# Optimization experiments

Hardware: AMD Instinct MI355X
Metric: run time of the kernel (lower is better)

The kernel has to match this reference:

```python
import jax, jax.numpy as jnp
import numpy as np

B, J, O = 32, 20, 20
D, H, F, L = 256, 8, 1024, 6
S = J * O
DH = D // H
NL = L + 1  # 6 encoder blocks + final block stacked together


def setup_inputs() -> dict:
    ks = jax.random.split(jax.random.key(0), 16)
    s = 0.02
    am = jax.random.randint(ks[4], (B, J), 0, 2) == 1
    am = am.at[:, 0].set(False)  # at least one unmasked job per row (avoid all -inf softmax)
    return {
        "operations": jax.random.normal(ks[0], (B, J, O, 2), jnp.float32),
        "job_ops_mask": jax.random.normal(ks[1], (B, J, O, O), jnp.float32),
        "ops_machines_mask": jax.random.normal(ks[2], (B, S, S), jnp.float32),
        "jobs_next_op_idx": jax.random.randint(ks[3], (B, J, 1), 0, O),
        "action_mask": am,
        "qkv_w": jax.random.normal(ks[5], (NL, 3 * D, D), jnp.float32) * s,
        "qkv_b": jnp.zeros((NL, 3 * D), jnp.float32),
        "out_w": jax.random.normal(ks[6], (NL, D, D), jnp.float32) * s,
        "out_b": jnp.zeros((NL, D), jnp.float32),
        "ln1_g": jnp.ones((NL, D), jnp.float32),
        "ln1_b": jnp.zeros((NL, D), jnp.float32),
        "ln2_g": jnp.ones((NL, D), jnp.float32),
        "ln2_b": jnp.zeros((NL, D), jnp.float32),
        "ff1_w": jax.random.normal(ks[7], (NL, F, D), jnp.float32) * s,
        "ff1_b": jnp.zeros((NL, F), jnp.float32),
        "ff2_w": jax.random.normal(ks[8], (NL, D, F), jnp.float32) * s,
        "ff2_b": jnp.zeros((NL, D), jnp.float32),
        "op_emb_w": jax.random.normal(ks[9], (D, 2), jnp.float32) * s,
        "op_emb_b": jnp.zeros((D,), jnp.float32),
        "pol_w": jax.random.normal(ks[10], (1, D), jnp.float32) * s,
        "pol_b": jnp.zeros((1,), jnp.float32),
    }


def _ln(x, g, b):
    m = x.mean(-1, keepdims=True)
    v = ((x - m) ** 2).mean(-1, keepdims=True)
    return (x - m) * jax.lax.rsqrt(v + 1e-5) * g + b


def _mha(x, mask, qw, qb, ow, ob):
    N, Sq, _ = x.shape
    qkv = x @ qw.T + qb
    q, k, v = jnp.split(qkv, 3, axis=-1)
    q = q.reshape(N, Sq, H, DH).transpose(0, 2, 1, 3)
    k = k.reshape(N, Sq, H, DH).transpose(0, 2, 1, 3)
    v = v.reshape(N, Sq, H, DH).transpose(0, 2, 1, 3)
    sc = jnp.einsum("nhqd,nhkd->nhqk", q, k) / jnp.sqrt(jnp.float32(DH))
    sc = sc + mask  # additive float attn mask, broadcast over heads where needed
    a = jax.nn.softmax(sc, axis=-1)
    o = jnp.einsum("nhqk,nhkd->nhqd", a, v).transpose(0, 2, 1, 3).reshape(N, Sq, D)
    return o @ ow.T + ob


def _forward(operations, job_ops_mask, ops_machines_mask, jobs_next_op_idx, action_mask,
             qkv_w, qkv_b, out_w, out_b, ln1_g, ln1_b, ln2_g, ln2_b,
             ff1_w, ff1_b, ff2_w, ff2_b, op_emb_w, op_emb_b, pol_w, pol_b):
    def block(x, mask, i):  # pre-norm TransformerEncoderLayer, gelu, dropout=0
        h = _ln(x, ln1_g[i], ln1_b[i])
        x = x + _mha(h, mask, qkv_w[i], qkv_b[i], out_w[i], out_b[i])
        h = _ln(x, ln2_g[i], ln2_b[i])
        ff = jax.nn.gelu(h @ ff1_w[i].T + ff1_b[i], approximate=False) @ ff2_w[i].T + ff2_b[i]
        return x + ff

    # sinusoidal positional encoding over the operation index
    pos = jnp.arange(O, dtype=jnp.float32)[:, None]
    div = jnp.exp(jnp.arange(0, D, 2, dtype=jnp.float32) * (-np.log(10000.0) / D))
    pe = jnp.stack([jnp.sin(pos * div), jnp.cos(pos * div)], axis=-1).reshape(O, D)
    x = operations @ op_emb_w.T + op_emb_b + pe[None, None]  # (B,J,O,D)

    # ALiBi slopes: 1/x^(i+1), x = 256^(1/H)
    base = (2.0 ** 8) ** (1.0 / H)
    slope = (1.0 / base ** jnp.arange(1, H + 1, dtype=jnp.float32))[None, :, None, None]
    job_mask = job_ops_mask.reshape(B * J, 1, O, O) * slope  # (B*J, H, O, O)
    mach_mask = ops_machines_mask[:, None, :, :]  # (B, 1, S, S), identical across heads

    for i in range(L):
        if i % 2 == 0:  # per-job attention over operations
            x = block(x.reshape(B * J, O, D), job_mask, i).reshape(B, J, O, D)
        else:  # per-machine attention over all operations
            x = block(x.reshape(B, S, D), mach_mask, i).reshape(B, J, O, D)

    idx = jnp.broadcast_to(jobs_next_op_idx[:, :, :, None], (B, J, 1, D))
    nxt = jnp.take_along_axis(x, idx, axis=2)[:, :, 0, :]  # (B, J, D)
    kp = jnp.where(action_mask, -jnp.inf, 0.0)[:, None, None, :]  # key padding mask
    nxt = block(nxt, kp, L)
    logits = (nxt @ pol_w.T + pol_b)[:, :, 0]
    return jnp.where(action_mask, -jnp.inf, logits)


def reference(operations, job_ops_mask, ops_machines_mask, jobs_next_op_idx, action_mask,
              qkv_w, qkv_b, out_w, out_b, ln1_g, ln1_b, ln2_g, ln2_b,
              ff1_w, ff1_b, ff2_w, ff2_b, op_emb_w, op_emb_b, pol_w, pol_b):
    return _forward(operations, job_ops_mask, ops_machines_mask, jobs_next_op_idx, action_mask,
                    qkv_w, qkv_b, out_w, out_b, ln1_g, ln1_b, ln2_g, ln2_b,
                    ff1_w, ff1_b, ff2_w, ff2_b, op_emb_w, op_emb_b, pol_w, pol_b)
```

## Files before the change

kernel.cpp:

```cpp
#include <hip/hip_runtime.h>
#include <math.h>

#define B_  32
#define J_  20
#define O_  20
#define S_  400
#define D_  256
#define H_  8
#define F_  1024
#define L_  6
#define T_  12800
#define T2_ 640

#define NEG_BIG (-1e30f)

typedef __attribute__((ext_vector_type(8))) short short8;
typedef __attribute__((ext_vector_type(4))) float f32x4;

__device__ __forceinline__ short f2b(float f) {
  union { float f; unsigned u; } c; c.f = f;
  unsigned r = (c.u + 0x7FFFu + ((c.u >> 16) & 1u)) >> 16;
  return (short)r;
}
__device__ __forceinline__ float b2f(short s) {
  union { unsigned u; float f; } c;
  c.u = ((unsigned)(unsigned short)s) << 16;
  return c.f;
}
__device__ __forceinline__ unsigned addpk(unsigned a, unsigned b) {
  union { unsigned u; float f; } x, y;
  x.u = a << 16;        y.u = b << 16;        float lo = x.f + y.f;
  x.u = a & 0xffff0000u; y.u = b & 0xffff0000u; float hi = x.f + y.f;
  return (unsigned)(unsigned short)f2b(lo) | ((unsigned)(unsigned short)f2b(hi) << 16);
}
__device__ __forceinline__ void async_copy16(const short* g, short* l) {
  __builtin_amdgcn_global_load_lds(
      (const __attribute__((address_space(1))) void*)g,
      (__attribute__((address_space(3))) void*)l, 16, 0, 0);
}

__global__ __launch_bounds__(256) void k_f2b4(
    const float* __restrict__ s0, short* __restrict__ d0,
    const float* __restrict__ s1, short* __restrict__ d1,
    const float* __restrict__ s2, short* __restrict__ d2,
    const float* __restrict__ s3, short* __restrict__ d3,
    const float* __restrict__ s4, short* __restrict__ d4)
{
  int bid = blockIdx.x;
  const float* src; short* dst; int base;
  if (bid < 672)        { src = s0; dst = d0; base = bid; }
  else if (bid < 896)   { src = s1; dst = d1; base = bid - 672; }
  else if (bid < 1792)  { src = s2; dst = d2; base = bid - 896; }
  else if (bid < 2688)  { src = s3; dst = d3; base = bid - 1792; }
  else                  { src = s4; dst = d4; base = bid - 2688; }
  int i = (base * 256 + threadIdx.x) * 8;
  float4 a = *(const float4*)(src + i);
  float4 b = *(const float4*)(src + i + 4);
  short8 o;
  o[0] = f2b(a.x); o[1] = f2b(a.y); o[2] = f2b(a.z); o[3] = f2b(a.w);
  o[4] = f2b(b.x); o[5] = f2b(b.y); o[6] = f2b(b.z); o[7] = f2b(b.w);
  *(short8*)(dst + i) = o;
}

__global__ __launch_bounds__(640) void k_maskconv(
    const void* __restrict__ am_raw, int* __restrict__ am_out)
{
  __shared__ int isInt32;
  const int tid = threadIdx.x;
  if (tid == 0) isInt32 = 1;
  __syncthreads();
  if (tid < 160) {
    int v = ((const int*)am_raw)[tid];
    if (v != 0 && v != 1) atomicAnd(&isInt32, 0);
  }
  __syncthreads();
  if (tid < 640) {
    int v;
    if (isInt32) v = ((const int*)am_raw)[tid] != 0;
    else         v = ((const unsigned char*)am_raw)[tid] != 0;
    am_out[tid] = v;
  }
}

__global__ __launch_bounds__(256) void k_embed(
    const float* __restrict__ ops, const float* __restrict__ ew,
    const float* __restrict__ eb, short* __restrict__ x)
{
  int idx = blockIdx.x * 256 + threadIdx.x;
  int d = idx & 255;
  int t = idx >> 8;
  int o = t % O_;
  float a0 = ops[(size_t)t * 2 + 0], a1 = ops[(size_t)t * 2 + 1];
  int k = d >> 1;
  float div = expf((float)(2 * k) * -0.03597789207803197f);
  float ang = (float)o * div;
  float pe = (d & 1) ? cosf(ang) : sinf(ang);
  x[idx] = f2b(a0 * ew[d * 2 + 0] + a1 * ew[d * 2 + 1] + eb[d] + pe);
}

__global__ __launch_bounds__(256) void k_ln(
    const short* __restrict__ x, const float* __restrict__ g, const float* __restrict__ b,
    short* __restrict__ out, int nTok)
{
  int gid = blockIdx.x * 256 + threadIdx.x;
  int tok = gid >> 6, lane = threadIdx.x & 63;
  if (tok >= nTok) return;
  int2 pk = ((const int2*)(x + (size_t)tok * 256))[lane];
  union { unsigned u; float f; } c;
  float vx, vy, vz, vw;
  c.u = (unsigned)pk.x << 16;        vx = c.f;
  c.u = (unsigned)pk.x & 0xffff0000u; vy = c.f;
  c.u = (unsigned)pk.y << 16;        vz = c.f;
  c.u = (unsigned)pk.y & 0xffff0000u; vw = c.f;
  float s = vx + vy + vz + vw;
  #pragma unroll
  for (int off = 32; off > 0; off >>= 1) s += __shfl_down(s, off);
  float mean = __shfl(s, 0) * (1.f / 256.f);
  float dx = vx - mean, dy = vy - mean, dz = vz - mean, dw = vw - mean;
  float q = dx * dx + dy * dy + dz * dz + dw * dw;
  #pragma unroll
  for (int off = 32; off > 0; off >>= 1) q += __shfl_down(q, off);
  float var = __shfl(q, 0) * (1.f / 256.f);
  float inv = 1.f / sqrtf(var + 1e-5f);
  float4 gv = ((const float4*)g)[lane];
  float4 bv = ((const float4*)b)[lane];
  float ox = dx * inv * gv.x + bv.x;
  float oy = dy * inv * gv.y + bv.y;
  float oz = dz * inv * gv.z + bv.z;
  float ow = dw * inv * gv.w + bv.w;
  int2 po;
  po.x = (int)(unsigned short)f2b(ox) | ((int)(unsigned short)f2b(oy) << 16);
  po.y = (int)(unsigned short)f2b(oz) | ((int)(unsigned short)f2b(ow) << 16);
  ((int2*)(out + (size_t)tok * 256))[lane] = po;
}

__global__ __launch_bounds__(256) void k_gemm_bf16(
    const short* __restrict__ A, const short* __restrict__ W,
    const float* __restrict__ bias, const short* __restrict__ R,
    short* __restrict__ C, int M, int N, int K, int act)
{
  __shared__ short LDS_[17408];
  short* Asf = LDS_;
  short* Bsf = LDS_ + 8192;
  short* Csf = LDS_;
  const int tid  = threadIdx.x;
  const int lane = tid & 63;
  const int wv   = tid >> 6;
  const int lm   = lane & 15;
  const int quad = lane >> 4;
  const int wm   = (wv >> 1) * 64;
  const int wn   = (wv & 1) * 64;
  const int n0 = blockIdx.x * 128;
  const int m0 = blockIdx.y * 128;

  f32x4 acc[4][4] = {};

  for (int k0 = 0; k0 < K; k0 += 64) {
    __syncthreads();
    #pragma unroll
    for (int i = 0; i < 4; ++i) {
      const int c    = tid + 256 * i;
      const int row  = c >> 3;
      const int kc8  = ((c & 7) ^ (row & 7)) * 8;
      async_copy16(A + (size_t)(m0 + row) * K + k0 + kc8, &Asf[c * 8]);
      async_copy16(W + (size_t)(n0 + row) * K + k0 + kc8, &Bsf[c * 8]);
    }
    __syncthreads();
    #pragma unroll
    for (int kh = 0; kh < 2; ++kh) {
      short8 af[4], bf[4];
      #pragma unroll
      for (int i = 0; i < 4; ++i) {
        const int row  = wm + i * 16 + lm;
        const int slot = (kh * 4 + quad) ^ (lm & 7);
        af[i] = *(short8*)&Asf[(row * 8 + slot) * 8];
      }
      #pragma unroll
      for (int j = 0; j < 4; ++j) {
        const int row  = wn + j * 16 + lm;
        const int slot = (kh * 4 + quad) ^ (lm & 7);
        bf[j] = *(short8*)&Bsf[(row * 8 + slot) * 8];
      }
      #pragma unroll
      for (int i = 0; i < 4; ++i)
        #pragma unroll
        for (int j = 0; j < 4; ++j)
          acc[i][j] = __builtin_amdgcn_mfma_f32_16x16x32_bf16(af[i], bf[j], acc[i][j], 0, 0, 0);
    }
  }

  __syncthreads();
  #pragma unroll
  for (int j = 0; j < 4; ++j) {
    const int ccol = wn + j * 16 + lm;
    const float bv = bias[n0 + ccol];
    #pragma unroll
    for (int i = 0; i < 4; ++i) {
      #pragma unroll
      for (int r = 0; r < 4; ++r) {
        const int row = wm + i * 16 + quad * 4 + r;
        float vvv = acc[i][j][r] + bv;
        if (act) vvv = vvv / (1.f + __expf(-1.702f * vvv));
        Csf[row * 136 + ccol] = f2b(vvv);
      }
    }
  }
  __syncthreads();
  {
    const int srow = tid >> 1, sh = (tid & 1) * 64;
    const size_t gbase = (size_t)(m0 + srow) * N + n0 + sh;
    const short* ls = &Csf[srow * 136 + sh];
    #pragma unroll
    for (int u = 0; u < 8; ++u) {
      uint4 v = *(const uint4*)(ls + u * 8);
      if (R) {
        uint4 rv = *(const uint4*)(R + gbase + u * 8);
        v.x = addpk(v.x, rv.x); v.y = addpk(v.y, rv.y);
        v.z = addpk(v.z, rv.z); v.w = addpk(v.w, rv.w);
      }
      *(uint4*)(C + gbase + u * 8) = v;
    }
  }
}

__global__ __launch_bounds__(256) void k_gemm_ln(
    const short* __restrict__ A, const short* __restrict__ W,
    const float* __restrict__ bias, const short* __restrict__ R,
    short* __restrict__ X, short* __restrict__ Hout,
    const float* __restrict__ g, const float* __restrict__ bb_,
    int M, int K)
{
  __shared__ short LDS_[4096 + 16896];
  short* Asf = LDS_;
  short* Bsf = LDS_ + 4096;
  short* Csf = LDS_ + 4096;
  const int tid  = threadIdx.x;
  const int lane = tid & 63;
  const int wv   = tid >> 6;
  const int lm   = lane & 15;
  const int quad = lane >> 4;
  const int wn   = wv * 64;
  const int m0   = blockIdx.x * 64;

  f32x4 acc[4][4] = {};

  for (int k0 = 0; k0 < K; k0 += 64) {
    __syncthreads();
    #pragma unroll
    for (int i = 0; i < 2; ++i) {
      const int c   = tid + 256 * i;
      const int row = c >> 3;
      const int kc8 = ((c & 7) ^ (row & 7)) * 8;
      async_copy16(A + (size_t)(m0 + row) * K + k0 + kc8, &Asf[c * 8]);
    }
    #pragma unroll
    for (int i = 0; i < 8; ++i) {
      const int c   = tid + 256 * i;
      const int row = c >> 3;
      const int kc8 = ((c & 7) ^ (row & 7)) * 8;
      async_copy16(W + (size_t)row * K + k0 + kc8, &Bsf[c * 8]);
    }
    __syncthreads();
    #pragma unroll
    for (int kh = 0; kh < 2; ++kh) {
      short8 af[4], bf[4];
      #pragma unroll
      for (int i = 0; i < 4; ++i) {
        const int row  = i * 16 + lm;
        const int slot = (kh * 4 + quad) ^ (lm & 7);
        af[i] = *(short8*)&Asf[(row * 8 + slot) * 8];
      }
      #pragma unroll
      for (int j = 0; j < 4; ++j) {
        const int row  = wn + j * 16 + lm;
        const int slot = (kh * 4 + quad) ^ (lm & 7);
        bf[j] = *(short8*)&Bsf[(row * 8 + slot) * 8];
      }
      #pragma unroll
      for (int i = 0; i < 4; ++i)
        #pragma unroll
        for (int j = 0; j < 4; ++j)
          acc[i][j] = __builtin_amdgcn_mfma_f32_16x16x32_bf16(af[i], bf[j], acc[i][j], 0, 0, 0);
    }
  }

  __syncthreads();
  #pragma unroll
  for (int j = 0; j < 4; ++j) {
    const int ccol = wn + j * 16 + lm;
    const float bv = bias[ccol];
    #pragma unroll
    for (int i = 0; i < 4; ++i) {
      #pragma unroll
      for (int r = 0; r < 4; ++r) {
        const int row = i * 16 + quad * 4 + r;
        Csf[row * 264 + ccol] = f2b(acc[i][j][r] + bv);
      }
    }
  }
  __syncthreads();

  {
    const int row = tid >> 2, cb = (tid & 3) * 64;
    const size_t gbase = (size_t)(m0 + row) * 256 + cb;
    const short* ls = &Csf[row * 264 + cb];
    uint4 xv[8];
    float s1 = 0.f, s2 = 0.f;
    #pragma unroll
    for (int u = 0; u < 8; ++u) {
      uint4 v = *(const uint4*)(ls + u * 8);
      uint4 rv = *(const uint4*)(R + gbase + u * 8);
      v.x = addpk(v.x, rv.x); v.y = addpk(v.y, rv.y);
      v.z = addpk(v.z, rv.z); v.w = addpk(v.w, rv.w);
      xv[u] = v;
      *(uint4*)(X + gbase + u * 8) = v;
      #pragma unroll
      for (int w2 = 0; w2 < 4; ++w2) {
        unsigned pv = (&v.x)[w2];
        union { unsigned u; float f; } c1, c2;
        c1.u = pv << 16; c2.u = pv & 0xffff0000u;
        s1 += c1.f + c2.f;
        s2 += c1.f * c1.f + c2.f * c2.f;
      }
    }
    s1 += __shfl_xor(s1, 1); s2 += __shfl_xor(s2, 1);
    s1 += __shfl_xor(s1, 2); s2 += __shfl_xor(s2, 2);
    const float mean = s1 * (1.f / 256.f);
    const float var  = s2 * (1.f / 256.f) - mean * mean;
    const float inv  = 1.f / sqrtf(var + 1e-5f);
    #pragma unroll
    for (int u = 0; u < 8; ++u) {
      float4 g0 = *(const float4*)(g + cb + u * 8);
      float4 g1 = *(const float4*)(g + cb + u * 8 + 4);
      float4 b0 = *(const float4*)(bb_ + cb + u * 8);
      float4 b1 = *(const float4*)(bb_ + cb + u * 8 + 4);
      auto lnpk = [&](unsigned pv, float ga, float gb2, float ba, float bb2) -> unsigned {
        union { unsigned u; float f; } c1, c2;
        c1.u = pv << 16; c2.u = pv & 0xffff0000u;
        float lo = (c1.f - mean) * inv * ga + ba;
        float hi = (c2.f - mean) * inv * gb2 + bb2;
        return (unsigned)(unsigned short)f2b(lo) | ((unsigned)(unsigned short)f2b(hi) << 16);
      };
      uint4 hv;
      hv.x = lnpk(xv[u].x, g0.x, g0.y, b0.x, b0.y);
      hv.y = lnpk(xv[u].y, g0.z, g0.w, b0.z, b0.w);
      hv.z = lnpk(xv[u].z, g1.x, g1.y, b1.x, b1.y);
      hv.w = lnpk(xv[u].w, g1.z, g1.w, b1.z, b1.w);
      *(uint4*)(Hout + gbase + u * 8) = hv;
    }
  }
}

#define QSTR 776
#define PSTR20 40
__global__ __launch_bounds__(512) void k_attn20_mfma(
    const short* __restrict__ qkv, short* __restrict__ att,
    const float* __restrict__ jmask, const int* __restrict__ amask, int mode)
{
  __shared__ short QK[32 * QSTR];
  __shared__ short Ps[8][32 * PSTR20];
  const int seq  = blockIdx.x;
  const int tid  = threadIdx.x;
  const int wv   = tid >> 6;
  const int lane = tid & 63;
  const int l15  = lane & 15;
  const int quad = lane >> 4;
  const float scale = 0.1767766952966369f;

  for (int e = tid; e < 3072; e += 512) {
    int row = e / 96, c8 = (e % 96) * 8;
    uint4 v = {0u, 0u, 0u, 0u};
    if (row < 20) v = *(const uint4*)(qkv + ((size_t)seq * 20 + row) * 768 + c8);
    *(uint4*)&QK[row * QSTR + c8] = v;
  }
  __syncthreads();

  const short8 aq0 = *(short8*)&QK[(0  + l15) * QSTR + wv * 32 + quad * 8];
  const short8 aq1 = *(short8*)&QK[(16 + l15) * QSTR + wv * 32 + quad * 8];
  const short8 bk0 = *(short8*)&QK[(0  + l15) * QSTR + 256 + wv * 32 + quad * 8];
  const short8 bk1 = *(short8*)&QK[(16 + l15) * QSTR + 256 + wv * 32 + quad * 8];
  f32x4 z4 = {0.f, 0.f, 0.f, 0.f};
  f32x4 s00 = __builtin_amdgcn_mfma_f32_16x16x32_bf16(aq0, bk0, z4, 0, 0, 0);
  f32x4 s01 = __builtin_amdgcn_mfma_f32_16x16x32_bf16(aq0, bk1, z4, 0, 0, 0);
  f32x4 s10 = __builtin_amdgcn_mfma_f32_16x16x32_bf16(aq1, bk0, z4, 0, 0, 0);
  f32x4 s11 = __builtin_amdgcn_mfma_f32_16x16x32_bf16(aq1, bk1, z4, 0, 0, 0);

  const float slope = exp2f(-(float)(wv + 1));
  short* psw = &Ps[wv][0];
  float l0[4] = {0.f, 0.f, 0.f, 0.f};
  float l1[4] = {0.f, 0.f, 0.f, 0.f};

  #pragma unroll
  for (int kt = 0; kt < 2; ++kt) {
    const int k  = kt * 16 + l15;
    const int kc = (k < 20) ? k : 19;
    float madd1 = 0.f;
    if (mode == 1) madd1 = amask[seq * 20 + kc] ? NEG_BIG : 0.f;
    #pragma unroll
    for (int qt = 0; qt < 2; ++qt) {
      f32x4 s = (kt == 0) ? (qt == 0 ? s00 : s10) : (qt == 0 ? s01 : s11);
      #pragma unroll
      for (int r = 0; r < 4; ++r) {
        const int q  = qt * 16 + quad * 4 + r;
        const int qc = (q < 20) ? q : 19;
        float sv = s[r] * scale;
        if (mode == 0) sv += jmask[(size_t)seq * 400 + qc * 20 + kc] * slope;
        else           sv += madd1;
        float p = (k < 20) ? __expf(fminf(sv, 40.f)) : 0.f;
        if (qt == 0) l0[r] += p; else l1[r] += p;
        psw[q * PSTR20 + k] = f2b(p);
      }
    }
  }
  #pragma unroll
  for (int r = 0; r < 4; ++r) {
    float t0 = l0[r];
    t0 += __shfl_xor(t0, 1); t0 += __shfl_xor(t0, 2);
    t0 += __shfl_xor(t0, 4); t0 += __shfl_xor(t0, 8);
    l0[r] = 1.f / t0;
    float t1 = l1[r];
    t1 += __shfl_xor(t1, 1); t1 += __shfl_xor(t1, 2);
    t1 += __shfl_xor(t1, 4); t1 += __shfl_xor(t1, 8);
    l1[r] = 1.f / t1;
  }

  const short8 pf0 = *(short8*)&psw[(0  + l15) * PSTR20 + quad * 8];
  const short8 pf1 = *(short8*)&psw[(16 + l15) * PSTR20 + quad * 8];
  #pragma unroll
  for (int dt = 0; dt < 2; ++dt) {
    const int d = wv * 32 + dt * 16 + l15;
    short8 vf;
    #pragma unroll
    for (int j = 0; j < 8; ++j)
      vf[j] = QK[(quad * 8 + j) * QSTR + 512 + d];
    f32x4 o0 = __builtin_amdgcn_mfma_f32_16x16x32_bf16(pf0, vf, z4, 0, 0, 0);
    f32x4 o1 = __builtin_amdgcn_mfma_f32_16x16x32_bf16(pf1, vf, z4, 0, 0, 0);
    #pragma unroll
    for (int r = 0; r < 4; ++r) {
      const int q = quad * 4 + r;
      att[((size_t)seq * 20 + q) * 256 + d] = f2b(o0[r] * l0[r]);
    }
    if (quad == 0) {
      #pragma unroll
      for (int r = 0; r < 4; ++r) {
        const int q = 16 + r;
        att[((size_t)seq * 20 + q) * 256 + d] = f2b(o1[r] * l1[r]);
      }
    }
  }
}

#define VTS 416
__global__ __launch_bounds__(256) void k_vtrans(
    const short* __restrict__ qkv, short* __restrict__ vt)
{
  __shared__ short T[64][73];
  const int bid = blockIdx.x;
  const int b  = bid / 28, rem = bid % 28;
  const int kt = rem / 4, dt = rem % 4;
  const int k0 = kt * 64, d0 = dt * 64;
  const int tid = threadIdx.x;
  #pragma unroll
  for (int i = 0; i < 2; ++i) {
    const int c = tid + 256 * i;
    const int row = c >> 3, cc = (c & 7) * 8;
    const int tok = k0 + row;
    uint4 v = {0u, 0u, 0u, 0u};
    if (tok < 400)
      v = *(const uint4*)(qkv + ((size_t)(b * 400 + tok)) * 768 + 512 + d0 + cc);
    *(uint4*)&T[row][cc] = v;
  }
  __syncthreads();
  #pragma unroll
  for (int i = 0; i < 2; ++i) {
    const int c = tid + 256 * i;
    const int dl = c >> 3, kk = (c & 7) * 8;
    if (k0 + kk < VTS) {
      short8 o;
      #pragma unroll
      for (int j = 0; j < 8; ++j) o[j] = T[kk + j][dl];
      *(short8*)(vt + ((size_t)(b * 256 + d0 + dl)) * VTS + k0 + kk) = o;
    }
  }
}

#define PSTRW 40
#define MSTR 424
__global__ __launch_bounds__(512) void k_attn400_mfma(
    const short* __restrict__ qkv, const short* __restrict__ vt,
    short* __restrict__ att, const short* __restrict__ mbf)
{
  __shared__ short Pl[8][2 * 16 * PSTRW];
  __shared__ short Ml[32 * MSTR];

  const int id   = blockIdx.x;
  const int b    = (id & 7) + 8 * ((id >> 3) / 13);
  const int qt   = (id >> 3) % 13;
  const int tid  = threadIdx.x;
  const int wv   = tid >> 6;
  const int lane = tid & 63;
  const int l15  = lane & 15;
  const int quad = lane >> 4;
  const int q0   = qt * 32;
  const float scale = 0.1767766952966369f;

  for (int e = tid; e < 32 * 52; e += 512) {
    const int row = e / 52, cc = e % 52;
    const int srow = (q0 + row < 400) ? (q0 + row) : 399;
    uint4 v = {0u, 0u, 0u, 0u};
    if (cc < 50)
      v = *(const uint4*)(mbf + ((size_t)(b * 400 + srow)) * 400 + cc * 8);
    *(uint4*)&Ml[row * MSTR + cc * 8] = v;
  }

  short* Pw0 = &Pl[wv][0];
  short* Pw1 = &Pl[wv][16 * PSTRW];
  const short* qbase = qkv + (size_t)b * 400 * 768;
  const short* vtb   = vt + ((size_t)b * 256 + wv * 32) * VTS;

  const short8 af0 = *(const short8*)(qbase + (size_t)(q0 + l15) * 768 + wv * 32 + quad * 8);
  int aq1 = q0 + 16 + l15; if (aq1 > 399) aq1 = 399;
  const short8 af1 = *(const short8*)(qbase + (size_t)aq1 * 768 + wv * 32 + quad * 8);

  f32x4 accO[2][2] = {};
  float lsum0 = 0.f, lsum1 = 0.f;

  short8 kA0, kA1, vA0, vA1, kB0, kB1, vB0, vB1;

#define PREFKV(K0, KF0, KF1, VF0, VF1)                                          \
  {                                                                             \
    KF0 = *(const short8*)(qbase + (size_t)((K0) + l15) * 768 + 256 + wv * 32 + quad * 8); \
    int kr_ = (K0) + 16 + l15; if (kr_ > 399) kr_ = 399;                        \
    KF1 = *(const short8*)(qbase + (size_t)kr_ * 768 + 256 + wv * 32 + quad * 8); \
    VF0 = *(const short8*)(vtb + (size_t)(0  + l15) * VTS + (K0) + quad * 8);   \
    VF1 = *(const short8*)(vtb + (size_t)(16 + l15) * VTS + (K0) + quad * 8);   \
  }

#define BODY(K0, KF0, KF1, VF0, VF1)                                            \
  {                                                                             \
    f32x4 z4 = {0.f, 0.f, 0.f, 0.f};                                            \
    f32x4 s00 = __builtin_amdgcn_mfma_f32_16x16x32_bf16(KF0, af0, z4, 0, 0, 0); \
    f32x4 s01 = __builtin_amdgcn_mfma_f32_16x16x32_bf16(KF1, af0, z4, 0, 0, 0); \
    f32x4 s10 = __builtin_amdgcn_mfma_f32_16x16x32_bf16(KF0, af1, z4, 0, 0, 0); \
    f32x4 s11 = __builtin_amdgcn_mfma_f32_16x16x32_bf16(KF1, af1, z4, 0, 0, 0); \
    const short* mr0 = &Ml[l15 * MSTR];                                         \
    const short* mr1 = &Ml[(16 + l15) * MSTR];                                  \
    uint2 ma0 = *(const uint2*)(mr0 + (K0) + quad * 4);                         \
    uint2 mb0 = *(const uint2*)(mr0 + (K0) + 16 + quad * 4);                    \
    uint2 ma1 = *(const uint2*)(mr1 + (K0) + quad * 4);                         \
    uint2 mb1 = *(const uint2*)(mr1 + (K0) + 16 + quad * 4);                    \
    float p00[4], p01[4], p10[4], p11[4];                                       \
    _Pragma("unroll")                                                           \
    for (int r = 0; r < 4; ++r) {                                               \
      const int kB = (K0) + 16 + quad * 4 + r;                                  \
      union { unsigned u; float f; } cm;                                        \
      unsigned wa0 = (r < 2) ? ma0.x : ma0.y;                                   \
      unsigned wb0 = (r < 2) ? mb0.x : mb0.y;                                   \
      unsigned wa1 = (r < 2) ? ma1.x : ma1.y;                                   \
      unsigned wb1 = (r < 2) ? mb1.x : mb1.y;                                   \
      cm.u = (r & 1) ? (wa0 & 0xffff0000u) : (wa0 << 16); float mA0 = cm.f;     \
      cm.u = (r & 1) ? (wb0 & 0xffff0000u) : (wb0 << 16); float mB0 = cm.f;     \
      cm.u = (r & 1) ? (wa1 & 0xffff0000u) : (wa1 << 16); float mA1 = cm.f;     \
      cm.u = (r & 1) ? (wb1 & 0xffff0000u) : (wb1 << 16); float mB1 = cm.f;     \
      float sA0 = s00[r] * scale + mA0;                                         \
      float sB0 = (kB < 400) ? (s01[r] * scale + mB0) : NEG_BIG;                \
      float sA1 = s10[r] * scale + mA1;                                         \
      float sB1 = (kB < 400) ? (s11[r] * scale + mB1) : NEG_BIG;                \
      p00[r] = __expf(fminf(sA0, 40.f));                                        \
      p01[r] = __expf(fminf(sB0, 40.f));                                        \
      p10[r] = __expf(fminf(sA1, 40.f));                                        \
      p11[r] = __expf(fminf(sB1, 40.f));                                        \
      lsum0 += p00[r] + p01[r];                                                 \
      lsum1 += p10[r] + p11[r];                                                 \
    }                                                                           \
    unsigned q00, q01, q02, q03, q10, q11, q12, q13;                            \
    asm("v_cvt_pk_bf16_f32 %0, %1, %2" : "=v"(q00) : "v"(p00[0]), "v"(p00[1]));  \
    asm("v_cvt_pk_bf16_f32 %0, %1, %2" : "=v"(q01) : "v"(p00[2]), "v"(p00[3]));  \
    asm("v_cvt_pk_bf16_f32 %0, %1, %2" : "=v"(q02) : "v"(p01[0]), "v"(p01[1]));  \
    asm("v_cvt_pk_bf16_f32 %0, %1, %2" : "=v"(q03) : "v"(p01[2]), "v"(p01[3]));  \
    asm("v_cvt_pk_bf16_f32 %0, %1, %2" : "=v"(q10) : "v"(p10[0]), "v"(p10[1]));  \
    asm("v_cvt_pk_bf16_f32 %0, %1, %2" : "=v"(q11) : "v"(p10[2]), "v"(p10[3]));  \
    asm("v_cvt_pk_bf16_f32 %0, %1, %2" : "=v"(q12) : "v"(p11[0]), "v"(p11[1]));  \
    asm("v_cvt_pk_bf16_f32 %0, %1, %2" : "=v"(q13) : "v"(p11[2]), "v"(p11[3]));  \
    uint2 w00; w00.x = q00; w00.y = q01;                                        \
    uint2 w01; w01.x = q02; w01.y = q03;                                        \
    uint2 w10; w10.x = q10; w10.y = q11;                                        \
    uint2 w11; w11.x = q12; w11.y = q13;                                        \
    *(uint2*)&Pw0[l15 * PSTRW + quad * 4]      = w00;                           \
    *(uint2*)&Pw0[l15 * PSTRW + 16 + quad * 4] = w01;                           \
    *(uint2*)&Pw1[l15 * PSTRW + quad * 4]      = w10;                           \
    *(uint2*)&Pw1[l15 * PSTRW + 16 + quad * 4] = w11;                           \
    const short8 pf0 = *(short8*)&Pw0[l15 * PSTRW + quad * 8];                  \
    const short8 pf1 = *(short8*)&Pw1[l15 * PSTRW + quad * 8];                  \
    accO[0][0] = __builtin_amdgcn_mfma_f32_16x16x32_bf16(VF0, pf0, accO[0][0], 0, 0, 0); \
    accO[0][1] = __builtin_amdgcn_mfma_f32_16x16x32_bf16(VF1, pf0, accO[0][1], 0, 0, 0); \
    accO[1][0] = __builtin_amdgcn_mfma_f32_16x16x32_bf16(VF0, pf1, accO[1][0], 0, 0, 0); \
    accO[1][1] = __builtin_amdgcn_mfma_f32_16x16x32_bf16(VF1, pf1, accO[1][1], 0, 0, 0); \
  }

  PREFKV(0, kA0, kA1, vA0, vA1)
  PREFKV(32, kB0, kB1, vB0, vB1)

  __syncthreads();

  int k0 = 0;
  #pragma unroll 1
  for (int it = 0; it < 6; ++it) {
    BODY(k0, kA0, kA1, vA0, vA1)
    if (k0 + 64 < 416) PREFKV(k0 + 64, kA0, kA1, vA0, vA1)
    k0 += 32;
    BODY(k0, kB0, kB1, vB0, vB1)
    if (k0 + 64 < 416) PREFKV(k0 + 64, kB0, kB1, vB0, vB1)
    k0 += 32;
  }
  BODY(k0, kA0, kA1, vA0, vA1)

#undef PREFKV
#undef BODY

  lsum0 += __shfl_xor(lsum0, 16);
  lsum0 += __shfl_xor(lsum0, 32);
  lsum1 += __shfl_xor(lsum1, 16);
  lsum1 += __shfl_xor(lsum1, 32);
  const float inv0 = 1.f / lsum0;
  const float inv1 = 1.f / lsum1;

  #pragma unroll
  for (int qh = 0; qh < 2; ++qh) {
    const int q = q0 + qh * 16 + l15;
    if (q >= 400) continue;
    const float inv = qh ? inv1 : inv0;
    #pragma unroll
    for (int c = 0; c < 2; ++c) {
      float a0 = accO[qh][c][0] * inv, a1 = accO[qh][c][1] * inv;
      float a2 = accO[qh][c][2] * inv, a3 = accO[qh][c][3] * inv;
      unsigned o01, o23;
      asm("v_cvt_pk_bf16_f32 %0, %1, %2" : "=v"(o01) : "v"(a0), "v"(a1));
      asm("v_cvt_pk_bf16_f32 %0, %1, %2" : "=v"(o23) : "v"(a2), "v"(a3));
      uint2 ov; ov.x = o01; ov.y = o23;
      *(uint2*)&att[((size_t)b * 400 + q) * 256 + wv * 32 + c * 16 + quad * 4] = ov;
    }
  }
}

__global__ __launch_bounds__(256) void k_gather2(
    const short* __restrict__ x, const short* __restrict__ h,
    const int* __restrict__ idx, short* __restrict__ x2, short* __restrict__ h2)
{
  int t = blockIdx.x * 256 + threadIdx.x;
  if (t >= 640 * 16) return;
  int bj = t >> 4, c = t & 15;
  int o = idx[bj];
  size_t src = ((size_t)bj * 20 + o) * 256;
  ((uint4*)(x2 + (size_t)bj * 256))[c] = ((const uint4*)(x + src))[c];
  ((uint4*)(h2 + (size_t)bj * 256))[c] = ((const uint4*)(h + src))[c];
}

__global__ __launch_bounds__(256) void k_logits(
    const short* __restrict__ x2, const float* __restrict__ pw, const float* __restrict__ pb,
    const int* __restrict__ am, float* __restrict__ out)
{
  int gid = blockIdx.x * 256 + threadIdx.x;
  int row = gid >> 6, lane = threadIdx.x & 63;
  int2 pk = ((const int2*)(x2 + (size_t)row * 256))[lane];
  union { unsigned u; float f; } c;
  float vx, vy, vz, vw;
  c.u = (unsigned)pk.x << 16;         vx = c.f;
  c.u = (unsigned)pk.x & 0xffff0000u; vy = c.f;
  c.u = (unsigned)pk.y << 16;         vz = c.f;
  c.u = (unsigned)pk.y & 0xffff0000u; vw = c.f;
  float4 w = ((const float4*)pw)[lane];
  float s = vx * w.x + vy * w.y + vz * w.z + vw * w.w;
  #pragma unroll
  for (int off = 32; off > 0; off >>= 1) s += __shfl_down(s, off);
  if (lane == 0) out[row] = am[row] ? NEG_BIG : (s + pb[0]);
}

extern "C" void kernel_launch(void* const* d_in, const int* in_sizes, int n_in,
                              void* d_out, int out_size, void* d_ws, size_t ws_size,
                              hipStream_t stream)
{
  (void)in_sizes; (void)n_in; (void)out_size; (void)ws_size;
  const float* operations        = (const float*)d_in[0];
  const float* job_ops_mask      = (const float*)d_in[1];
  const float* ops_machines_mask = (const float*)d_in[2];
  const int*   jobs_next_op_idx  = (const int*)d_in[3];
  const void*  action_mask_raw   = (const void*)d_in[4];
  const float* qkv_w = (const float*)d_in[5];
  const float* qkv_b = (const float*)d_in[6];
  const float* out_w = (const float*)d_in[7];
  const float* out_b = (const float*)d_in[8];
  const float* ln1_g = (const float*)d_in[9];
  const float* ln1_b = (const float*)d_in[10];
  const float* ln2_g = (const float*)d_in[11];
  const float* ln2_b = (const float*)d_in[12];
  const float* ff1_w = (const float*)d_in[13];
  const float* ff1_b = (const float*)d_in[14];
  const float* ff2_w = (const float*)d_in[15];
  const float* ff2_b = (const float*)d_in[16];
  const float* op_emb_w = (const float*)d_in[17];
  const float* op_emb_b = (const float*)d_in[18];
  const float* pol_w = (const float*)d_in[19];
  const float* pol_b = (const float*)d_in[20];
  float* out = (float*)d_out;

  short* x    = (short*)d_ws;
  short* x2   = x + (size_t)T_ * D_;
  short* h    = x2 + (size_t)T2_ * D_;
  short* big  = h + (size_t)T_ * D_;
  short* h2   = big + (size_t)T_ * F_;
  short* big2 = h2 + (size_t)T2_ * D_;
  int*   amc  = (int*)(big2 + (size_t)T2_ * F_);
  short* bwq  = (short*)(amc + 640);
  short* bwo  = bwq + (size_t)7 * 768 * 256;
  short* bwf1 = bwo + (size_t)7 * 256 * 256;
  short* bwf2 = bwf1 + (size_t)7 * 1024 * 256;
  short* mbf  = bwf2 + (size_t)7 * 256 * 1024;
  short* vt   = mbf + (size_t)B_ * 400 * 400;

  auto gemm = [&](const short* A, const short* Wb, const float* bias, const short* R,
                  short* C, int M, int N, int K, int act) {
    k_gemm_bf16<<<dim3(N / 128, M / 128), dim3(256), 0, stream>>>(
        A, Wb, bias, R, C, M, N, K, act);
  };
  auto gemm_ln = [&](const short* A, const short* Wb, const float* bias, const short* R,
                     short* X, short* Hout, const float* g, const float* b, int M, int K) {
    k_gemm_ln<<<dim3(M / 64), dim3(256), 0, stream>>>(
        A, Wb, bias, R, X, Hout, g, b, M, K);
  };

  k_f2b4<<<dim3(5188), 256, 0, stream>>>(qkv_w, bwq, out_w, bwo, ff1_w, bwf1,
                                         ff2_w, bwf2, ops_machines_mask, mbf);
  k_maskconv<<<dim3(1), dim3(640), 0, stream>>>(action_mask_raw, amc);
  k_embed<<<dim3(T_ * D_ / 256), dim3(256), 0, stream>>>(operations, op_emb_w, op_emb_b, x);
  k_ln<<<dim3(T_ / 4), 256, 0, stream>>>(x, ln1_g, ln1_b, h, T_);

  for (int i = 0; i < L_; ++i) {
    const short* qw  = bwq  + (size_t)i * 768 * 256;
    const float* qb  = qkv_b + (size_t)i * 768;
    const short* ow  = bwo  + (size_t)i * 256 * 256;
    const float* ob  = out_b + (size_t)i * 256;
    const short* f1w = bwf1 + (size_t)i * 1024 * 256;
    const float* f1b = ff1_b + (size_t)i * 1024;
    const short* f2w = bwf2 + (size_t)i * 256 * 1024;
    const float* f2b_ = ff2_b + (size_t)i * 256;
    gemm(h, qw, qb, nullptr, big, T_, 768, 256, 0);
    if ((i & 1) == 0) {
      k_attn20_mfma<<<dim3(640), 512, 0, stream>>>(big, h, job_ops_mask, nullptr, 0);
    } else {
      k_vtrans<<<dim3(896), 256, 0, stream>>>(big, vt);
      k_attn400_mfma<<<dim3(416), 512, 0, stream>>>(big, vt, h, mbf);
    }
    gemm_ln(h, ow, ob, x, x, h, ln2_g + i * D_, ln2_b + i * D_, T_, 256);
    gemm(h, f1w, f1b, nullptr, big, T_, 1024, 256, 1);
    gemm_ln(big, f2w, f2b_, x, x, h, ln1_g + (i + 1) * D_, ln1_b + (i + 1) * D_, T_, 1024);
  }

  k_gather2<<<dim3(40), 256, 0, stream>>>(x, h, jobs_next_op_idx, x2, h2);

  {
    int i = L_;
    const short* qw  = bwq  + (size_t)i * 768 * 256;
    const float* qb  = qkv_b + (size_t)i * 768;
    const short* ow  = bwo  + (size_t)i * 256 * 256;
    const float* ob  = out_b + (size_t)i * 256;
    const short* f1w = bwf1 + (size_t)i * 1024 * 256;
    const float* f1b = ff1_b + (size_t)i * 1024;
    const short* f2w = bwf2 + (size_t)i * 256 * 1024;
    const float* f2b_ = ff2_b + (size_t)i * 256;
    gemm(h2, qw, qb, nullptr, big2, T2_, 768, 256, 0);
    k_attn20_mfma<<<dim3(32), 512, 0, stream>>>(big2, h2, nullptr, amc, 1);
    gemm_ln(h2, ow, ob, x2, x2, h2, ln2_g + i * D_, ln2_b + i * D_, T2_, 256);
    gemm(h2, f1w, f1b, nullptr, big2, T2_, 1024, 256, 1);
    gemm(big2, f2w, f2b_, x2, x2, T2_, 256, 1024, 0);
  }

  k_logits<<<dim3(160), 256, 0, stream>>>(x2, pol_w, pol_b, amc, out);
}
```

Before: 931.9 us.

## Double-buffer LDS tiles in bf16 GEMM and GEMM+LayerNorm kernels

Both GEMM kernels now keep two LDS stages. The next K-tile's async global-to-LDS copy is issued before the MFMA work on the current tile, and each iteration uses one barrier instead of two. The aim is to hide global load latency behind matrix math. In exchange, LDS per block roughly doubles (64 KB and 80 KB), which lowers how many blocks can be resident per CU.

```diff
diff --git a/kernel.cpp b/kernel.cpp
--- a/kernel.cpp
+++ b/kernel.cpp
@@ -139,9 +139,7 @@
     const float* __restrict__ bias, const short* __restrict__ R,
     short* __restrict__ C, int M, int N, int K, int act)
 {
-  __shared__ short LDS_[17408];
-  short* Asf = LDS_;
-  short* Bsf = LDS_ + 8192;
+  __shared__ short LDS_[32768];
   short* Csf = LDS_;
   const int tid  = threadIdx.x;
   const int lane = tid & 63;
@@ -155,17 +153,27 @@
 
   f32x4 acc[4][4] = {};
 
-  for (int k0 = 0; k0 < K; k0 += 64) {
-    __syncthreads();
-    #pragma unroll
-    for (int i = 0; i < 4; ++i) {
-      const int c    = tid + 256 * i;
-      const int row  = c >> 3;
-      const int kc8  = ((c & 7) ^ (row & 7)) * 8;
-      async_copy16(A + (size_t)(m0 + row) * K + k0 + kc8, &Asf[c * 8]);
-      async_copy16(W + (size_t)(n0 + row) * K + k0 + kc8, &Bsf[c * 8]);
-    }
-    __syncthreads();
+#define GB_STAGE(buf, kk)                                                      \
+  { _Pragma("unroll")                                                          \
+    for (int i = 0; i < 4; ++i) {                                              \
+      const int c    = tid + 256 * i;                       \
+      const int row  = c >> 3;                                     \
+      const int kc8  = ((c & 7) ^ (row & 7)) * 8;                              \
+      async_copy16(A + (size_t)(m0 + row) * K + (kk) + kc8,                    \
+                   &LDS_[(buf) * 16384 + c * 8]);                              \
+      async_copy16(W + (size_t)(n0 + row) * K + (kk) + kc8,                    \
+                   &LDS_[(buf) * 16384 + 8192 + c * 8]);                       \
+    } }
+
+  GB_STAGE(0, 0)
+  __syncthreads();
+
+  const int nIter = K >> 6;
+  for (int t = 0; t < nIter; ++t) {
+    const int cur = t & 1;
+    if (t + 1 < nIter) GB_STAGE(cur ^ 1, (t + 1) << 6)
+    const short* Asf = &LDS_[cur * 16384];
+    const short* Bsf = &LDS_[cur * 16384 + 8192];
     #pragma unroll
     for (int kh = 0; kh < 2; ++kh) {
       short8 af[4], bf[4];
@@ -187,9 +195,10 @@
         for (int j = 0; j < 4; ++j)
           acc[i][j] = __builtin_amdgcn_mfma_f32_16x16x32_bf16(af[i], bf[j], acc[i][j], 0, 0, 0);
     }
-  }
-
-  __syncthreads();
+    __syncthreads();
+  }
+#undef GB_STAGE
+
   #pragma unroll
   for (int j = 0; j < 4; ++j) {
     const int ccol = wn + j * 16 + lm;
@@ -230,10 +239,8 @@
     const float* __restrict__ g, const float* __restrict__ bb_,
     int M, int K)
 {
-  __shared__ short LDS_[4096 + 16896];
-  short* Asf = LDS_;
-  short* Bsf = LDS_ + 4096;
-  short* Csf = LDS_ + 4096;
+  __shared__ short LDS_[40960];
+  short* Csf = LDS_;
   const int tid  = threadIdx.x;
   const int lane = tid & 63;
   const int wv   = tid >> 6;
@@ -244,23 +251,33 @@
 
   f32x4 acc[4][4] = {};
 
-  for (int k0 = 0; k0 < K; k0 += 64) {
-    __syncthreads();
-    #pragma unroll
-    for (int i = 0; i < 2; ++i) {
-      const int c   = tid + 256 * i;
-      const int row = c >> 3;
-      const int kc8 = ((c & 7) ^ (row & 7)) * 8;
-      async_copy16(A + (size_t)(m0 + row) * K + k0 + kc8, &Asf[c * 8]);
-    }
-    #pragma unroll
-    for (int i = 0; i < 8; ++i) {
-      const int c   = tid + 256 * i;
-      const int row = c >> 3;
-      const int kc8 = ((c & 7) ^ (row & 7)) * 8;
-      async_copy16(W + (size_t)row * K + k0 + kc8, &Bsf[c * 8]);
-    }
-    __syncthreads();
+#define GL_STAGE(buf, kk)                                                      \
+  { _Pragma("unroll")                                                          \
+    for (int i = 0; i < 2; ++i) {                           \
+      const int c   = tid + 256 * i;                                           \
+      const int row = c >> 3;                                                  \
+      const int kc8 = ((c & 7) ^ (row & 7)) * 8;                               \
+      async_copy16(A + (size_t)(m0 + row) * K + (kk) + kc8,                    \
+                   &LDS_[(buf) * 20480 + c * 8]);                              \
+    }                                                                          \
+    _Pragma("unroll")                                                          \
+    for (int i = 0; i < 8; ++i) {           \
+      const int c   = tid + 256 * i;                                           \
+      const int row = c >> 3;                                                  \
+      const int kc8 = ((c & 7) ^ (row & 7)) * 8;                               \
+      async_copy16(W + (size_t)row * K + (kk) + kc8,                           \
+                   &LDS_[(buf) * 20480 + 4096 + c * 8]);                       \
+    } }
+
+  GL_STAGE(0, 0)
+  __syncthreads();
+
+  const int nIter = K >> 6;
+  for (int t = 0; t < nIter; ++t) {
+    const int cur = t & 1;
+    if (t + 1 < nIter) GL_STAGE(cur ^ 1, (t + 1) << 6)
+    const short* Asf = &LDS_[cur * 20480];
+    const short* Bsf = &LDS_[cur * 20480 + 4096];
     #pragma unroll
     for (int kh = 0; kh < 2; ++kh) {
       short8 af[4], bf[4];
@@ -282,9 +299,10 @@
         for (int j = 0; j < 4; ++j)
           acc[i][j] = __builtin_amdgcn_mfma_f32_16x16x32_bf16(af[i], bf[j], acc[i][j], 0, 0, 0);
     }
-  }
-
-  __syncthreads();
+    __syncthreads();
+  }
+#undef GL_STAGE
+
   #pragma unroll
   for (int j = 0; j < 4; ++j) {
     const int ccol = wn + j * 16 + lm;
```

Result: faster. 876.7 us (-5.9%).
